# Optimization experiments

Measured on AMD Instinct MI355X. Metric: run time of the kernel, lower is better.

Reference implementation:

```python
import jax, jax.numpy as jnp
import numpy as np

NUM_FIELDS = 40
EMBED_DIM = 16

# Precompute static gather indices equivalent to the two masked_select calls.
# triu mask on a (F, F-1) grid, diagonal=0 -> pairs (i, j) with j >= i.
_tri = np.triu(np.ones((NUM_FIELDS, NUM_FIELDS - 1), dtype=np.int64), 0).astype(bool)
_I0, _J0 = np.nonzero(_tri)  # row-major order matches torch.masked_select
# tril(ones(F, F-1), -1).T -> (F-1, F) mask applied to x.transpose(1, 2).
_trl = np.tril(np.ones((NUM_FIELDS, NUM_FIELDS - 1), dtype=np.int64), -1).T.astype(bool)
_I1, _J1 = np.nonzero(_trl)  # indices into the transposed view
I0 = jnp.asarray(_I0); J0 = jnp.asarray(_J0)
I1 = jnp.asarray(_I1); J1 = jnp.asarray(_J1)


def setup_inputs() -> dict:
    key = jax.random.key(0)
    bs = 2048
    inputs = jax.random.normal(key, (bs, NUM_FIELDS * (NUM_FIELDS - 1) * EMBED_DIM), dtype=jnp.float32)
    return {"inputs": inputs}


def reference(inputs):
    bs = inputs.shape[0]
    F = NUM_FIELDS
    # [bs, F, F-1, D]
    x = inputs.reshape(bs, F, F - 1, -1)
    # emb0 = masked_select(x, triu_mask): gather pairs in row-major order
    emb0 = x[:, I0, J0, :]            # [bs, P, D], P = F*(F-1)/2
    # emb1 = masked_select(x.transpose(1,2), tril_mask): xt[b,a,c,:] = x[b,c,a,:]
    emb1 = x[:, J1, I1, :]            # [bs, P, D]
    # (emb0*emb1).view(bs,-1).sum(-1)
    return jnp.einsum('bpd,bpd->b', emb0, emb1)
```

## Files before the change

### kernel.cpp

```cpp
#include <hip/hip_runtime.h>


#define NPAIRS 780
#define ROW_FLOATS 24960
#define NTASKS (NPAIRS * 4)

struct PairTab {
    unsigned short o0[NPAIRS];
    unsigned short o1[NPAIRS];
};

static constexpr PairTab make_tab() {
    PairTab t{};
    int p = 0;
    for (int i = 0; i < 39; ++i) {
        for (int j = i; j < 39; ++j, ++p) {
            t.o0[p] = (unsigned short)(i * 39 + j);
            t.o1[p] = (unsigned short)((j + 1) * 39 + i);
        }
    }
    return t;
}

__constant__ PairTab c_tab = make_tab();

__global__ __launch_bounds__(256) void ffm_interact_kernel(
        const float* __restrict__ x, float* __restrict__ out) {
    const int n = blockIdx.x;
    const float4* __restrict__ base4 =
        (const float4*)(x + (size_t)n * ROW_FLOATS);

    float acc = 0.0f;
    for (int task = threadIdx.x; task < NTASKS; task += 256) {
        const int p = task >> 2;
        const int q = task & 3;
        const float4 a = base4[(int)c_tab.o0[p] * 4 + q];
        const float4 b = base4[(int)c_tab.o1[p] * 4 + q];
        acc = fmaf(a.x, b.x, acc);
        acc = fmaf(a.y, b.y, acc);
        acc = fmaf(a.z, b.z, acc);
        acc = fmaf(a.w, b.w, acc);
    }

    #pragma unroll
    for (int off = 32; off > 0; off >>= 1)
        acc += __shfl_down(acc, off, 64);

    __shared__ float wave_sum[4];
    const int lane = threadIdx.x & 63;
    const int wid  = threadIdx.x >> 6;
    if (lane == 0) wave_sum[wid] = acc;
    __syncthreads();
    if (threadIdx.x == 0)
        out[n] = wave_sum[0] + wave_sum[1] + wave_sum[2] + wave_sum[3];
}

extern "C" void kernel_launch(void* const* d_in, const int* in_sizes, int n_in,
                              void* d_out, int out_size, void* d_ws, size_t ws_size,
                              hipStream_t stream) {
    const float* x = (const float*)d_in[0];
    float* out = (float*)d_out;
    const int bs = in_sizes[0] / ROW_FLOATS;
    ffm_interact_kernel<<<bs, 256, 0, stream>>>(x, out);
}
```

Before: 280.3 us.

## Stage lower-triangle vectors in LDS with coalesced loads and use 512 threads

```diff
diff --git a/kernel.cpp b/kernel.cpp
--- a/kernel.cpp
+++ b/kernel.cpp
@@ -1,41 +1,60 @@
 #include <hip/hip_runtime.h>
 
 
+#define NF 40
+#define NC 39
+#define ED 16
 #define NPAIRS 780
-#define ROW_FLOATS 24960
+#define ROW_FLOATS (NF * NC * ED)
 #define NTASKS (NPAIRS * 4)
+#define NTHREADS 512
 
-struct PairTab {
-    unsigned short o0[NPAIRS];
-    unsigned short o1[NPAIRS];
+struct Tables {
+    unsigned short a_glob[NPAIRS];
+    unsigned short b_slot[NPAIRS];
+    unsigned short b_glob[NPAIRS];
 };
 
-static constexpr PairTab make_tab() {
-    PairTab t{};
+static constexpr Tables make_tables() {
+    Tables t{};
     int p = 0;
-    for (int i = 0; i < 39; ++i) {
-        for (int j = i; j < 39; ++j, ++p) {
-            t.o0[p] = (unsigned short)(i * 39 + j);
-            t.o1[p] = (unsigned short)((j + 1) * 39 + i);
+    for (int i = 0; i < NC; ++i)
+        for (int j = i; j < NC; ++j, ++p) {
+            t.a_glob[p] = (unsigned short)(i * NC + j);
+            t.b_slot[p] = (unsigned short)((j + 1) * j / 2 + i);
         }
-    }
+    for (int g = 1; g < NF; ++g)
+        for (int c = 0; c < g; ++c)
+            t.b_glob[g * (g - 1) / 2 + c] = (unsigned short)(g * NC + c);
     return t;
 }
 
-__constant__ PairTab c_tab = make_tab();
+__constant__ Tables c_tab = make_tables();
 
-__global__ __launch_bounds__(256) void ffm_interact_kernel(
+__global__ __launch_bounds__(NTHREADS) void ffm_interact_kernel(
         const float* __restrict__ x, float* __restrict__ out) {
+    __shared__ float ldsb[NPAIRS * ED];
     const int n = blockIdx.x;
+    const int tid = threadIdx.x;
     const float4* __restrict__ base4 =
         (const float4*)(x + (size_t)n * ROW_FLOATS);
+    float4* lds4 = (float4*)ldsb;
+
+    #pragma unroll
+    for (int t = tid; t < NTASKS; t += NTHREADS) {
+        const int s = t >> 2;
+        const int q = t & 3;
+        lds4[s * 4 + q] = base4[(int)c_tab.b_glob[s] * 4 + q];
+    }
+    __syncthreads();
 
     float acc = 0.0f;
-    for (int task = threadIdx.x; task < NTASKS; task += 256) {
-        const int p = task >> 2;
-        const int q = task & 3;
-        const float4 a = base4[(int)c_tab.o0[p] * 4 + q];
-        const float4 b = base4[(int)c_tab.o1[p] * 4 + q];
+    #pragma unroll
+    for (int t = tid; t < NTASKS; t += NTHREADS) {
+        const int p = t >> 2;
+        const int q = t & 3;
+        const float4 a = base4[(int)c_tab.a_glob[p] * 4 + q];
+        const float4 b = lds4[(int)c_tab.b_slot[p] * 4 + q];
         acc = fmaf(a.x, b.x, acc);
         acc = fmaf(a.y, b.y, acc);
         acc = fmaf(a.z, b.z, acc);
@@ -46,13 +65,17 @@
     for (int off = 32; off > 0; off >>= 1)
         acc += __shfl_down(acc, off, 64);
 
-    __shared__ float wave_sum[4];
+    __shared__ float wave_sum[NTHREADS / 64];
     const int lane = threadIdx.x & 63;
     const int wid  = threadIdx.x >> 6;
     if (lane == 0) wave_sum[wid] = acc;
     __syncthreads();
-    if (threadIdx.x == 0)
-        out[n] = wave_sum[0] + wave_sum[1] + wave_sum[2] + wave_sum[3];
+    if (tid == 0) {
+        float s = 0.0f;
+        #pragma unroll
+        for (int w = 0; w < NTHREADS / 64; ++w) s += wave_sum[w];
+        out[n] = s;
+    }
 }
 
 extern "C" void kernel_launch(void* const* d_in, const int* in_sizes, int n_in,
@@ -61,5 +84,5 @@
     const float* x = (const float*)d_in[0];
     float* out = (float*)d_out;
     const int bs = in_sizes[0] / ROW_FLOATS;
-    ffm_interact_kernel<<<bs, 256, 0, stream>>>(x, out);
+    ffm_interact_kernel<<<bs, NTHREADS, 0, stream>>>(x, out);
 }
```

Result: no change. 274.9 us (-1.9%).
